# Performance work log

Measured on AMD Instinct MI355X. Metric: run time of the kernel, lower is better.

The kernel has to match this reference:

```python
import jax, jax.numpy as jnp
import numpy as np


def setup_inputs() -> dict:
    key = jax.random.key(0)
    k0, k1, k2, k3 = jax.random.split(key, 4)
    T, H, I, E, K = 2048, 2048, 1408, 8, 2  # tokens, hidden, intermediate, experts, top-k
    hidden_states = jax.random.normal(k0, (T, H), dtype=jnp.float32)
    router_weight = jax.random.normal(k1, (H, E), dtype=jnp.float32) * 0.02
    gate_up_weight = jax.random.normal(k2, (E, H, 2 * I), dtype=jnp.float32) * 0.02
    down_weight = jax.random.normal(k3, (E, I, H), dtype=jnp.float32) * 0.02
    return {
        "hidden_states": hidden_states,
        "router_weight": router_weight,
        "gate_up_weight": gate_up_weight,
        "down_weight": down_weight,
        "top_k": K,
    }


def reference(hidden_states, router_weight, gate_up_weight, down_weight, top_k):
    # Router: logits -> softmax -> top-k -> renormalize ('normalization' path)
    router_logits = hidden_states @ router_weight                  # [T, E]
    router_weights = jax.nn.softmax(router_logits, axis=-1)       # [T, E]
    topk_w, topk_idx = jax.lax.top_k(router_weights, top_k)       # [T, K]
    topk_w = topk_w / jnp.sum(topk_w, axis=-1, keepdims=True)     # router_weights_topk_reduced

    T, H = hidden_states.shape
    I = down_weight.shape[1]

    # Grouped gate_up GEMM (dense-per-expert reference for the grouped GMM)
    gate_up = jnp.einsum('th,ehf->etf', hidden_states, gate_up_weight)  # [E, T, 2I]
    gate, up = gate_up[..., :I], gate_up[..., I:]
    swish_out = jax.nn.silu(gate) * up                              # SWIGLU  [E, T, I]
    mlp_out = jnp.einsum('eti,eih->eth', swish_out, down_weight)    # [E, T, H]

    # Scatter-combine: gather each token's top-k expert outputs, weighted sum
    sel = mlp_out[topk_idx, jnp.arange(T)[:, None]]                 # [T, K, H]
    out = jnp.sum(sel * topk_w[..., None], axis=1)                  # [T, H]
    return out
```

## Files before the change

kernel.cpp:

```cpp
#include <hip/hip_runtime.h>
#include <hip/hip_bf16.h>
#include <math.h>

#define T_TOK 2048
#define HDIM  2048
#define IDIM  1408
#define NG    2816
#define NEXP  8
#define NPAIR (T_TOK*2)
#define RPAD  6144

typedef __attribute__((ext_vector_type(4))) float  f32x4;
typedef __attribute__((ext_vector_type(4))) short  s16x4;
typedef __attribute__((ext_vector_type(8))) short  s16x8;
typedef __attribute__((ext_vector_type(8))) __bf16 bf16x8;

__device__ __forceinline__ short f2bf(float f) {
  union { float f; unsigned u; } v; v.f = f;
  unsigned r = v.u + 0x7FFFu + ((v.u >> 16) & 1u);
  return (short)(r >> 16);
}

__device__ __forceinline__ float bf2f(short s) {
  union { unsigned u; float f; } v; v.u = ((unsigned)(unsigned short)s) << 16;
  return v.f;
}

__device__ __forceinline__ void gload_lds16(const void* g, void* l) {
  __builtin_amdgcn_global_load_lds((const __attribute__((address_space(1))) unsigned int*)g,
                                   (__attribute__((address_space(3))) unsigned int*)l,
                                   16, 0, 0);
}

__global__ void router_kernel(const float* __restrict__ hs, const float* __restrict__ rw,
                              int* __restrict__ pair_e, float* __restrict__ pair_w,
                              int* __restrict__ pair_pos, int* __restrict__ counts) {
  int wid = threadIdx.x >> 6, lane = threadIdx.x & 63;
  int t = blockIdx.x * 4 + wid;
  float acc[NEXP];
#pragma unroll
  for (int e = 0; e < NEXP; e++) acc[e] = 0.f;
  const float* h = hs + (size_t)t * HDIM;
  for (int k = lane; k < HDIM; k += 64) {
    float x = h[k];
    f32x4 w0 = *(const f32x4*)(rw + (size_t)k * NEXP);
    f32x4 w1 = *(const f32x4*)(rw + (size_t)k * NEXP + 4);
#pragma unroll
    for (int e = 0; e < 4; e++) { acc[e] += x * w0[e]; acc[e + 4] += x * w1[e]; }
  }
#pragma unroll
  for (int e = 0; e < NEXP; e++)
#pragma unroll
    for (int off = 32; off > 0; off >>= 1)
      acc[e] += __shfl_xor(acc[e], off, 64);
  if (lane == 0) {
    int i1 = 0; float v1 = acc[0];
#pragma unroll
    for (int e = 1; e < NEXP; e++) if (acc[e] > v1) { v1 = acc[e]; i1 = e; }
    int i2 = -1; float v2 = -3.4e38f;
#pragma unroll
    for (int e = 0; e < NEXP; e++) if (e != i1 && acc[e] > v2) { v2 = acc[e]; i2 = e; }
    float w2 = 1.f / (1.f + expf(v1 - v2));
    float w1 = 1.f - w2;
    int p1 = atomicAdd(&counts[i1], 1);
    int p2 = atomicAdd(&counts[i2], 1);
    pair_e[2*t]   = i1; pair_w[2*t]   = w1; pair_pos[2*t]   = p1;
    pair_e[2*t+1] = i2; pair_w[2*t+1] = w2; pair_pos[2*t+1] = p2;
  }
}

__global__ void prefix_kernel(const int* __restrict__ counts, int* __restrict__ offs) {
  if (threadIdx.x == 0) {
    int s = 0;
    for (int e = 0; e < NEXP; e++) { offs[e] = s; s += (counts[e] + 255) & ~255; }
    offs[NEXP] = s;
  }
}

__global__ void rowmap_kernel(const int* __restrict__ pair_e, const float* __restrict__ pair_w,
                              const int* __restrict__ pair_pos, const int* __restrict__ offs,
                              int* __restrict__ row_token, float* __restrict__ row_weight,
                              int* __restrict__ tok2row) {
  int p = blockIdx.x * 256 + threadIdx.x;
  if (p >= NPAIR) return;
  int e = pair_e[p];
  int row = offs[e] + pair_pos[p];
  row_token[row] = p >> 1;
  row_weight[row] = pair_w[p];
  tok2row[p] = row;
}

__global__ __launch_bounds__(256) void gather_kernel(const float* __restrict__ hs,
                                                     const int* __restrict__ row_token,
                                                     short* __restrict__ A_c) {
  int r = blockIdx.x;
  int tok = row_token[r];
  int t = threadIdx.x;
  if (tok < 0) {
    *(s16x8*)&A_c[(size_t)r * HDIM + t * 8] = (s16x8)0;
    return;
  }
  const float* src = hs + (size_t)tok * HDIM + t * 8;
  f32x4 v0 = *(const f32x4*)src;
  f32x4 v1 = *(const f32x4*)(src + 4);
  s16x8 o;
#pragma unroll
  for (int j = 0; j < 4; j++) { o[j] = f2bf(v0[j]); o[4 + j] = f2bf(v1[j]); }
  int dstg = (t & ~7) | ((t & 7) ^ (r & 7));
  *(s16x8*)&A_c[(size_t)r * HDIM + dstg * 8] = o;
}

__global__ __launch_bounds__(256) void convert_w_kernel(
    const float* __restrict__ src, short* __restrict__ dst, int K, int N) {
  int e = blockIdx.z;
  src += (size_t)e * K * N;
  dst += (size_t)e * K * N;
  int n0 = blockIdx.x * 64, k0 = blockIdx.y * 64;
  __shared__ short tile[64 * 76];
  int tid = threadIdx.x;
#pragma unroll
  for (int it = 0; it < 4; it++) {
    int s = tid + it * 256;
    int kk = s >> 4, nn = (s & 15) * 4;
    f32x4 v = *(const f32x4*)(src + (size_t)(k0 + kk) * N + n0 + nn);
    s16x4 b;
#pragma unroll
    for (int j = 0; j < 4; j++) b[j] = f2bf(v[j]);
    *(s16x4*)&tile[kk * 76 + nn] = b;
  }
  __syncthreads();
#pragma unroll
  for (int it = 0; it < 2; it++) {
    int s = tid + it * 256;
    int n = s >> 3, g = s & 7;
    int gs = g ^ (n & 7);
    s16x8 o;
#pragma unroll
    for (int j = 0; j < 8; j++) o[j] = tile[(gs * 8 + j) * 76 + n];
    *(s16x8*)&dst[(size_t)(n0 + n) * K + k0 + g * 8] = o;
  }
}

__global__ __launch_bounds__(512, 2) void gateup_kernel(
    const short* __restrict__ A_c, const float* __restrict__ guw,
    const int* __restrict__ offs, short* __restrict__ S) {
  int nb = blockIdx.x;
  int rb = blockIdx.y * 256;
  if (rb >= offs[NEXP]) return;
  int e = 0;
#pragma unroll
  for (int i = 1; i < NEXP; i++) e += (rb >= offs[i]);
  const float* Wsrc = guw + (size_t)e * HDIM * NG;
  const short* Ar = A_c + (size_t)rb * HDIM;

  __shared__ short bufA[2][256 * 64];
  __shared__ short bufB[256 * 64];
  int tid = threadIdx.x, lane = tid & 63, wid = tid >> 6;
  int wm = wid >> 2, wn = wid & 3;
  int lm = lane & 15, lg = lane >> 4;

  int oct = tid >> 4, kq = tid & 15;
  int n0 = oct * 8;
  int col = (n0 < 128) ? (nb * 128 + n0) : (IDIM + nb * 128 + (n0 - 128));
  const float* Bp = Wsrc + col;

  f32x4 acc[8][4];
#pragma unroll
  for (int a = 0; a < 8; a++)
#pragma unroll
    for (int b = 0; b < 4; b++) acc[a][b] = (f32x4)0.f;

  f32x4 va[4], vb[4];

  auto STAGE_A = [&](int buf, int kt) {
    int k0 = kt * 64;
#pragma unroll
    for (int it = 0; it < 4; it++) {
      int idx = tid + it * 512;
      gload_lds16(Ar + (size_t)(idx >> 3) * HDIM + k0 + (idx & 7) * 8, &bufA[buf][idx * 8]);
    }
  };
  auto LOAD_B = [&](int kt) {
    const float* p = Bp + (size_t)(kt * 64 + kq * 4) * NG;
#pragma unroll
    for (int j = 0; j < 4; j++) {
      va[j] = *(const f32x4*)(p + (size_t)j * NG);
      vb[j] = *(const f32x4*)(p + (size_t)j * NG + 4);
    }
  };
  auto WRITE_B = [&]() {
    int gc = kq >> 1, half = kq & 1;
#pragma unroll
    for (int i = 0; i < 8; i++) {
      int n = n0 + i;
      s16x4 w;
#pragma unroll
      for (int j = 0; j < 4; j++) w[j] = f2bf(i < 4 ? va[j][i] : vb[j][i - 4]);
      *(s16x4*)&bufB[n * 64 + ((gc ^ (n & 7)) * 8) + half * 4] = w;
    }
  };

  STAGE_A(0, 0);
  LOAD_B(0);
  const int NT = HDIM / 64;
#pragma unroll 1
  for (int kt = 0; kt < NT; kt++) {
    int cur = kt & 1;
    if (kt + 1 < NT) {
      STAGE_A(cur ^ 1, kt + 1);
      asm volatile("s_waitcnt vmcnt(4)" ::: "memory");
    } else {
      asm volatile("s_waitcnt vmcnt(0)" ::: "memory");
    }
    WRITE_B();
    if (kt + 1 < NT) LOAD_B(kt + 1);
    asm volatile("s_waitcnt lgkmcnt(0)" ::: "memory");
    __builtin_amdgcn_s_barrier();
#pragma unroll
    for (int ks = 0; ks < 2; ks++) {
      bf16x8 a[8], b[4];
#pragma unroll
      for (int mi = 0; mi < 8; mi++) {
        int m = wm * 128 + mi * 16 + lm;
        a[mi] = *(const bf16x8*)&bufA[cur][m * 64 + (((ks * 4 + lg) ^ (m & 7)) * 8)];
      }
#pragma unroll
      for (int nf = 0; nf < 4; nf++) {
        int n = (nf >> 1) * 128 + wn * 32 + (nf & 1) * 16 + lm;
        b[nf] = *(const bf16x8*)&bufB[n * 64 + (((ks * 4 + lg) ^ (n & 7)) * 8)];
      }
      __builtin_amdgcn_s_setprio(1);
#pragma unroll
      for (int mi = 0; mi < 8; mi++)
#pragma unroll
        for (int nf = 0; nf < 4; nf++)
          acc[mi][nf] = __builtin_amdgcn_mfma_f32_16x16x32_bf16(a[mi], b[nf], acc[mi][nf], 0, 0, 0);
      __builtin_amdgcn_s_setprio(0);
    }
    asm volatile("s_waitcnt lgkmcnt(0)" ::: "memory");
    __builtin_amdgcn_s_barrier();
  }
#pragma unroll
  for (int mi = 0; mi < 8; mi++)
#pragma unroll
    for (int nfg = 0; nfg < 2; nfg++)
#pragma unroll
      for (int j = 0; j < 4; j++) {
        int row = wm * 128 + mi * 16 + lg * 4 + j;
        int rg = rb + row;
        int scol = nb * 128 + wn * 32 + nfg * 16 + lm;
        int base = scol & ~63, o = scol & 63;
        int dc = (((o >> 3) ^ (rg & 7)) << 3) | (o & 7);
        float g = acc[mi][nfg][j], u = acc[mi][nfg + 2][j];
        float sv = (g / (1.f + expf(-g))) * u;
        S[(size_t)rg * IDIM + base + dc] = f2bf(sv);
      }
}

__global__ __launch_bounds__(512, 2) void down_kernel(
    const short* __restrict__ S, const short* __restrict__ W,
    const int* __restrict__ offs, short* __restrict__ Sout) {
  int nb = blockIdx.x;
  int rb = blockIdx.y * 256;
  if (rb >= offs[NEXP]) return;
  int e = 0;
#pragma unroll
  for (int i = 1; i < NEXP; i++) e += (rb >= offs[i]);
  const short* Ar = S + (size_t)rb * IDIM;
  const short* Bw = W + (size_t)e * HDIM * IDIM + (size_t)(nb * 256) * IDIM;

  __shared__ short As[2][256 * 64];
  __shared__ short Bs[2][256 * 64];
  int tid = threadIdx.x, lane = tid & 63, wid = tid >> 6;
  int wm = wid >> 2, wn = wid & 3;
  int lm = lane & 15, lg = lane >> 4;

  f32x4 acc[8][4];
#pragma unroll
  for (int a = 0; a < 8; a++)
#pragma unroll
    for (int b = 0; b < 4; b++) acc[a][b] = (f32x4)0.f;

  auto STAGE = [&](int buf, int kt) {
    int k0 = kt * 64;
#pragma unroll
    for (int it = 0; it < 4; it++) {
      int idx = tid + it * 512;
      gload_lds16(Ar + (size_t)(idx >> 3) * IDIM + k0 + (idx & 7) * 8, &As[buf][idx * 8]);
      gload_lds16(Bw + (size_t)(idx >> 3) * IDIM + k0 + (idx & 7) * 8, &Bs[buf][idx * 8]);
    }
  };
  auto READ_A = [&](bf16x8* dst, int buf, int mih, int ks) {
#pragma unroll
    for (int mi4 = 0; mi4 < 4; mi4++) {
      int m = wm * 128 + (mih * 4 + mi4) * 16 + lm;
      dst[mi4] = *(const bf16x8*)&As[buf][m * 64 + (((ks * 4 + lg) ^ (m & 7)) * 8)];
    }
  };
  auto READ_B = [&](bf16x8* dst, int buf, int ks) {
#pragma unroll
    for (int nf = 0; nf < 4; nf++) {
      int rbq = wn * 64 + nf * 16 + lm;
      dst[nf] = *(const bf16x8*)&Bs[buf][rbq * 64 + (((ks * 4 + lg) ^ (rbq & 7)) * 8)];
    }
  };
  auto MFMA16 = [&](const bf16x8* a, const bf16x8* b, int mih) {
    __builtin_amdgcn_s_setprio(1);
#pragma unroll
    for (int mi4 = 0; mi4 < 4; mi4++)
#pragma unroll
      for (int nf = 0; nf < 4; nf++)
        acc[mih * 4 + mi4][nf] =
            __builtin_amdgcn_mfma_f32_16x16x32_bf16(a[mi4], b[nf], acc[mih * 4 + mi4][nf], 0, 0, 0);
    __builtin_amdgcn_s_setprio(0);
  };

  STAGE(0, 0);
  const int NT = IDIM / 64;
#pragma unroll 1
  for (int kt = 0; kt < NT; kt++) {
    int cur = kt & 1;
    bf16x8 a0[4], a1[4], b0[4], b1[4];
    if (kt + 1 < NT) {
      STAGE(cur ^ 1, kt + 1);
      asm volatile("s_waitcnt vmcnt(8)" ::: "memory");
    } else {
      asm volatile("s_waitcnt vmcnt(0)" ::: "memory");
    }
    __builtin_amdgcn_s_barrier();
    READ_A(a0, cur, 0, 0); READ_B(b0, cur, 0);
    MFMA16(a0, b0, 0);
    READ_A(a1, cur, 1, 0);
    __builtin_amdgcn_s_barrier();
    MFMA16(a1, b0, 1);
    READ_A(a0, cur, 0, 1); READ_B(b1, cur, 1);
    __builtin_amdgcn_s_barrier();
    MFMA16(a0, b1, 0);
    READ_A(a1, cur, 1, 1);
    __builtin_amdgcn_s_barrier();
    MFMA16(a1, b1, 1);
    __builtin_amdgcn_s_barrier();
  }
#pragma unroll
  for (int mi = 0; mi < 8; mi++)
#pragma unroll
    for (int nf = 0; nf < 4; nf++)
#pragma unroll
      for (int j = 0; j < 4; j++) {
        int row = wm * 128 + mi * 16 + lg * 4 + j;
        int col = nb * 256 + wn * 64 + nf * 16 + lm;
        Sout[(size_t)(rb + row) * HDIM + col] = f2bf(acc[mi][nf][j]);
      }
}

__global__ __launch_bounds__(256) void combine_kernel(
    const short* __restrict__ Sout, const int* __restrict__ tok2row,
    const float* __restrict__ row_weight, float* __restrict__ out) {
  int t = blockIdx.x;
  int r1 = tok2row[2 * t], r2 = tok2row[2 * t + 1];
  float w1 = row_weight[r1], w2 = row_weight[r2];
  int c = threadIdx.x * 8;
  s16x8 a = *(const s16x8*)&Sout[(size_t)r1 * HDIM + c];
  s16x8 b = *(const s16x8*)&Sout[(size_t)r2 * HDIM + c];
  float* o = out + (size_t)t * HDIM + c;
#pragma unroll
  for (int j = 0; j < 8; j++) o[j] = w1 * bf2f(a[j]) + w2 * bf2f(b[j]);
}

extern "C" void kernel_launch(void* const* d_in, const int* in_sizes, int n_in,
                              void* d_out, int out_size, void* d_ws, size_t ws_size,
                              hipStream_t stream) {
  const float* hs  = (const float*)d_in[0];
  const float* rw  = (const float*)d_in[1];
  const float* guw = (const float*)d_in[2];
  const float* dw  = (const float*)d_in[3];
  float* out = (float*)d_out;

  char* ws = (char*)d_ws;
  size_t off = 0;
  auto take = [&](size_t b) { size_t p = off; off = (off + b + 255) & ~(size_t)255; return p; };
  size_t s_off      = take((size_t)RPAD * IDIM * 2);
  int*   counts     = (int*)(ws + take(32 * 4));
  int*   offs       = (int*)(ws + take(16 * 4));
  int*   pair_e     = (int*)(ws + take(NPAIR * 4));
  float* pair_w     = (float*)(ws + take(NPAIR * 4));
  int*   pair_pos   = (int*)(ws + take(NPAIR * 4));
  int*   row_token  = (int*)(ws + take(RPAD * 4));
  float* row_weight = (float*)(ws + take(RPAD * 4));
  int*   tok2row    = (int*)(ws + take(NPAIR * 4));
  size_t ac_off     = take((size_t)RPAD * HDIM * 2);
  size_t sout_off   = take((size_t)RPAD * HDIM * 2);
  size_t wd_off     = take((size_t)NEXP * HDIM * IDIM * 2);

  short* S    = (short*)(ws + s_off);
  short* A_c  = (short*)(ws + ac_off);
  short* Sout = (short*)(ws + sout_off);
  short* Wd   = (short*)(ws + wd_off);

  hipMemsetAsync(counts, 0, 32 * 4, stream);
  hipMemsetAsync(row_token, 0xFF, RPAD * 4, stream);

  router_kernel<<<T_TOK / 4, 256, 0, stream>>>(hs, rw, pair_e, pair_w, pair_pos, counts);
  prefix_kernel<<<1, 64, 0, stream>>>(counts, offs);
  rowmap_kernel<<<NPAIR / 256, 256, 0, stream>>>(pair_e, pair_w, pair_pos, offs,
                                                 row_token, row_weight, tok2row);
  gather_kernel<<<RPAD, 256, 0, stream>>>(hs, row_token, A_c);

  gateup_kernel<<<dim3(11, RPAD / 256), 512, 0, stream>>>(A_c, guw, offs, S);
  convert_w_kernel<<<dim3(HDIM / 64, IDIM / 64, NEXP), 256, 0, stream>>>(dw, Wd, IDIM, HDIM);
  down_kernel<<<dim3(8, RPAD / 256), 512, 0, stream>>>(S, Wd, offs, Sout);
  combine_kernel<<<T_TOK, 256, 0, stream>>>(Sout, tok2row, row_weight, out);
}
```

Measured before the change: 289.0 us.

## Fuse down-weight conversion into gate-up GEMM launch to overlap work

Measured after the change: 309.7 us. +7.1%, slower.

```diff
diff --git a/kernel.cpp b/kernel.cpp
--- a/kernel.cpp
+++ b/kernel.cpp
@@ -9,6 +9,9 @@
 #define NEXP  8
 #define NPAIR (T_TOK*2)
 #define RPAD  6144
+#define NB_GU   264
+#define NB_CVT  176
+#define CVT_TILES 32
 
 typedef __attribute__((ext_vector_type(4))) float  f32x4;
 typedef __attribute__((ext_vector_type(4))) short  s16x4;
@@ -110,42 +113,52 @@
   *(s16x8*)&A_c[(size_t)r * HDIM + dstg * 8] = o;
 }
 
-__global__ __launch_bounds__(256) void convert_w_kernel(
-    const float* __restrict__ src, short* __restrict__ dst, int K, int N) {
-  int e = blockIdx.z;
-  src += (size_t)e * K * N;
-  dst += (size_t)e * K * N;
-  int n0 = blockIdx.x * 64, k0 = blockIdx.y * 64;
-  __shared__ short tile[64 * 76];
+__global__ __launch_bounds__(512, 2) void gateup_cvt_kernel(
+    const short* __restrict__ A_c, const float* __restrict__ guw,
+    const float* __restrict__ dw, const int* __restrict__ offs,
+    short* __restrict__ S, short* __restrict__ Wd) {
+  __shared__ short bufA[2][256 * 64];
+  __shared__ short bufB[256 * 64];
+  int bid = blockIdx.x;
   int tid = threadIdx.x;
-#pragma unroll
-  for (int it = 0; it < 4; it++) {
-    int s = tid + it * 256;
-    int kk = s >> 4, nn = (s & 15) * 4;
-    f32x4 v = *(const f32x4*)(src + (size_t)(k0 + kk) * N + n0 + nn);
-    s16x4 b;
-#pragma unroll
-    for (int j = 0; j < 4; j++) b[j] = f2bf(v[j]);
-    *(s16x4*)&tile[kk * 76 + nn] = b;
-  }
-  __syncthreads();
-#pragma unroll
-  for (int it = 0; it < 2; it++) {
-    int s = tid + it * 256;
-    int n = s >> 3, g = s & 7;
-    int gs = g ^ (n & 7);
-    s16x8 o;
-#pragma unroll
-    for (int j = 0; j < 8; j++) o[j] = tile[(gs * 8 + j) * 76 + n];
-    *(s16x8*)&dst[(size_t)(n0 + n) * K + k0 + g * 8] = o;
-  }
-}
-
-__global__ __launch_bounds__(512, 2) void gateup_kernel(
-    const short* __restrict__ A_c, const float* __restrict__ guw,
-    const int* __restrict__ offs, short* __restrict__ S) {
-  int nb = blockIdx.x;
-  int rb = blockIdx.y * 256;
+
+  if (bid >= NB_GU) {
+    int c = bid - NB_GU;
+#pragma unroll 1
+    for (int i = 0; i < CVT_TILES; i++) {
+      int t = c * CVT_TILES + i;
+      int e = t / (32 * 22);
+      int rem = t % (32 * 22);
+      int ty = rem / 32, tx = rem % 32;
+      int k0 = ty * 64, n0 = tx * 64;
+      const float* src = dw + (size_t)e * IDIM * HDIM;
+#pragma unroll
+      for (int it = 0; it < 2; it++) {
+        int s = tid + it * 512;
+        int kk = s >> 4, nn = (s & 15) * 4;
+        f32x4 v = *(const f32x4*)(src + (size_t)(k0 + kk) * HDIM + n0 + nn);
+        s16x4 b;
+#pragma unroll
+        for (int j = 0; j < 4; j++) b[j] = f2bf(v[j]);
+        *(s16x4*)&bufB[kk * 76 + nn] = b;
+      }
+      __syncthreads();
+      {
+        int n = tid >> 3, g = tid & 7;
+        int gs = g ^ (n & 7);
+        s16x8 o;
+#pragma unroll
+        for (int j = 0; j < 8; j++) o[j] = bufB[(gs * 8 + j) * 76 + n];
+        *(s16x8*)&Wd[((size_t)e * HDIM + n0 + n) * IDIM + k0 + g * 8] = o;
+      }
+      __syncthreads();
+    }
+    return;
+  }
+
+  int nb = bid % 11;
+  int rblk = bid / 11;
+  int rb = rblk * 256;
   if (rb >= offs[NEXP]) return;
   int e = 0;
 #pragma unroll
@@ -153,9 +166,7 @@
   const float* Wsrc = guw + (size_t)e * HDIM * NG;
   const short* Ar = A_c + (size_t)rb * HDIM;
 
-  __shared__ short bufA[2][256 * 64];
-  __shared__ short bufB[256 * 64];
-  int tid = threadIdx.x, lane = tid & 63, wid = tid >> 6;
+  int lane = tid & 63, wid = tid >> 6;
   int wm = wid >> 2, wn = wid & 3;
   int lm = lane & 15, lg = lane >> 4;
 
@@ -406,8 +417,7 @@
                                                  row_token, row_weight, tok2row);
   gather_kernel<<<RPAD, 256, 0, stream>>>(hs, row_token, A_c);
 
-  gateup_kernel<<<dim3(11, RPAD / 256), 512, 0, stream>>>(A_c, guw, offs, S);
-  convert_w_kernel<<<dim3(HDIM / 64, IDIM / 64, NEXP), 256, 0, stream>>>(dw, Wd, IDIM, HDIM);
+  gateup_cvt_kernel<<<NB_GU + NB_CVT, 512, 0, stream>>>(A_c, guw, dw, offs, S, Wd);
   down_kernel<<<dim3(8, RPAD / 256), 512, 0, stream>>>(S, Wd, offs, Sout);
   combine_kernel<<<T_TOK, 256, 0, stream>>>(Sout, tok2row, row_weight, out);
 }
```

## Merge prefix into rowmap, fuse gather with weight convert, remap GEMM grids

Applied to the files above, without the earlier changes.

Measured after the change: 387.9 us. +34.2%, slower.

```diff
diff --git a/kernel.cpp b/kernel.cpp
--- a/kernel.cpp
+++ b/kernel.cpp
@@ -9,6 +9,7 @@
 #define NEXP  8
 #define NPAIR (T_TOK*2)
 #define RPAD  6144
+#define NCVT  (32*22*NEXP)
 
 typedef __attribute__((ext_vector_type(4))) float  f32x4;
 typedef __attribute__((ext_vector_type(4))) short  s16x4;
@@ -69,60 +70,66 @@
   }
 }
 
-__global__ void prefix_kernel(const int* __restrict__ counts, int* __restrict__ offs) {
+__global__ __launch_bounds__(256) void rowmap2_kernel(
+    const int* __restrict__ counts, const int* __restrict__ pair_e,
+    const float* __restrict__ pair_w, const int* __restrict__ pair_pos,
+    int* __restrict__ offs, int* __restrict__ row_token,
+    float* __restrict__ row_weight, int* __restrict__ tok2row) {
+  __shared__ int soffs[NEXP];
   if (threadIdx.x == 0) {
     int s = 0;
-    for (int e = 0; e < NEXP; e++) { offs[e] = s; s += (counts[e] + 255) & ~255; }
-    offs[NEXP] = s;
-  }
-}
-
-__global__ void rowmap_kernel(const int* __restrict__ pair_e, const float* __restrict__ pair_w,
-                              const int* __restrict__ pair_pos, const int* __restrict__ offs,
-                              int* __restrict__ row_token, float* __restrict__ row_weight,
-                              int* __restrict__ tok2row) {
+    for (int e = 0; e < NEXP; e++) { soffs[e] = s; s += (counts[e] + 255) & ~255; }
+    if (blockIdx.x == 0) {
+      for (int e = 0; e < NEXP; e++) offs[e] = soffs[e];
+      offs[NEXP] = s;
+    }
+  }
+  __syncthreads();
   int p = blockIdx.x * 256 + threadIdx.x;
   if (p >= NPAIR) return;
   int e = pair_e[p];
-  int row = offs[e] + pair_pos[p];
+  int row = soffs[e] + pair_pos[p];
   row_token[row] = p >> 1;
   row_weight[row] = pair_w[p];
   tok2row[p] = row;
 }
 
-__global__ __launch_bounds__(256) void gather_kernel(const float* __restrict__ hs,
-                                                     const int* __restrict__ row_token,
-                                                     short* __restrict__ A_c) {
-  int r = blockIdx.x;
-  int tok = row_token[r];
-  int t = threadIdx.x;
-  if (tok < 0) {
-    *(s16x8*)&A_c[(size_t)r * HDIM + t * 8] = (s16x8)0;
+__global__ __launch_bounds__(256) void gather_cvt_kernel(
+    const float* __restrict__ hs, const int* __restrict__ row_token,
+    short* __restrict__ A_c, const float* __restrict__ dw,
+    short* __restrict__ Wd) {
+  __shared__ short tile[64 * 76];
+  int bid = blockIdx.x, t = threadIdx.x;
+
+  if (bid < RPAD) {
+    int r = bid;
+    int tok = row_token[r];
+    if (tok < 0) {
+      *(s16x8*)&A_c[(size_t)r * HDIM + t * 8] = (s16x8)0;
+      return;
+    }
+    const float* src = hs + (size_t)tok * HDIM + t * 8;
+    f32x4 v0 = *(const f32x4*)src;
+    f32x4 v1 = *(const f32x4*)(src + 4);
+    s16x8 o;
+#pragma unroll
+    for (int j = 0; j < 4; j++) { o[j] = f2bf(v0[j]); o[4 + j] = f2bf(v1[j]); }
+    int dstg = (t & ~7) | ((t & 7) ^ (r & 7));
+    *(s16x8*)&A_c[(size_t)r * HDIM + dstg * 8] = o;
     return;
   }
-  const float* src = hs + (size_t)tok * HDIM + t * 8;
-  f32x4 v0 = *(const f32x4*)src;
-  f32x4 v1 = *(const f32x4*)(src + 4);
-  s16x8 o;
-#pragma unroll
-  for (int j = 0; j < 4; j++) { o[j] = f2bf(v0[j]); o[4 + j] = f2bf(v1[j]); }
-  int dstg = (t & ~7) | ((t & 7) ^ (r & 7));
-  *(s16x8*)&A_c[(size_t)r * HDIM + dstg * 8] = o;
-}
-
-__global__ __launch_bounds__(256) void convert_w_kernel(
-    const float* __restrict__ src, short* __restrict__ dst, int K, int N) {
-  int e = blockIdx.z;
-  src += (size_t)e * K * N;
-  dst += (size_t)e * K * N;
-  int n0 = blockIdx.x * 64, k0 = blockIdx.y * 64;
-  __shared__ short tile[64 * 76];
-  int tid = threadIdx.x;
+
+  int cid = bid - RPAD;
+  int e = cid / (32 * 22);
+  int rem = cid % (32 * 22);
+  int k0 = (rem / 32) * 64, n0 = (rem % 32) * 64;
+  const float* src = dw + (size_t)e * IDIM * HDIM;
+  short* dst = Wd + (size_t)e * IDIM * HDIM;
 #pragma unroll
   for (int it = 0; it < 4; it++) {
-    int s = tid + it * 256;
+    int s = t + it * 256;
     int kk = s >> 4, nn = (s & 15) * 4;
-    f32x4 v = *(const f32x4*)(src + (size_t)(k0 + kk) * N + n0 + nn);
+    f32x4 v = *(const f32x4*)(src + (size_t)(k0 + kk) * HDIM + n0 + nn);
     s16x4 b;
 #pragma unroll
     for (int j = 0; j < 4; j++) b[j] = f2bf(v[j]);
@@ -131,21 +138,22 @@
   __syncthreads();
 #pragma unroll
   for (int it = 0; it < 2; it++) {
-    int s = tid + it * 256;
+    int s = t + it * 256;
     int n = s >> 3, g = s & 7;
     int gs = g ^ (n & 7);
     s16x8 o;
 #pragma unroll
     for (int j = 0; j < 8; j++) o[j] = tile[(gs * 8 + j) * 76 + n];
-    *(s16x8*)&dst[(size_t)(n0 + n) * K + k0 + g * 8] = o;
+    *(s16x8*)&dst[(size_t)(n0 + n) * IDIM + k0 + g * 8] = o;
   }
 }
 
 __global__ __launch_bounds__(512, 2) void gateup_kernel(
     const short* __restrict__ A_c, const float* __restrict__ guw,
     const int* __restrict__ offs, short* __restrict__ S) {
-  int nb = blockIdx.x;
-  int rb = blockIdx.y * 256;
+  int bid = blockIdx.x;
+  int rblk = bid % 24, nb = bid / 24;
+  int rb = rblk * 256;
   if (rb >= offs[NEXP]) return;
   int e = 0;
 #pragma unroll
@@ -260,8 +268,9 @@
 __global__ __launch_bounds__(512, 2) void down_kernel(
     const short* __restrict__ S, const short* __restrict__ W,
     const int* __restrict__ offs, short* __restrict__ Sout) {
-  int nb = blockIdx.x;
-  int rb = blockIdx.y * 256;
+  int bid = blockIdx.x;
+  int rblk = bid % 24, nb = bid / 24;
+  int rb = rblk * 256;
   if (rb >= offs[NEXP]) return;
   int e = 0;
 #pragma unroll
@@ -401,13 +410,11 @@
   hipMemsetAsync(row_token, 0xFF, RPAD * 4, stream);
 
   router_kernel<<<T_TOK / 4, 256, 0, stream>>>(hs, rw, pair_e, pair_w, pair_pos, counts);
-  prefix_kernel<<<1, 64, 0, stream>>>(counts, offs);
-  rowmap_kernel<<<NPAIR / 256, 256, 0, stream>>>(pair_e, pair_w, pair_pos, offs,
-                                                 row_token, row_weight, tok2row);
-  gather_kernel<<<RPAD, 256, 0, stream>>>(hs, row_token, A_c);
-
-  gateup_kernel<<<dim3(11, RPAD / 256), 512, 0, stream>>>(A_c, guw, offs, S);
-  convert_w_kernel<<<dim3(HDIM / 64, IDIM / 64, NEXP), 256, 0, stream>>>(dw, Wd, IDIM, HDIM);
-  down_kernel<<<dim3(8, RPAD / 256), 512, 0, stream>>>(S, Wd, offs, Sout);
+  rowmap2_kernel<<<NPAIR / 256, 256, 0, stream>>>(counts, pair_e, pair_w, pair_pos,
+                                                  offs, row_token, row_weight, tok2row);
+  gather_cvt_kernel<<<RPAD + NCVT, 256, 0, stream>>>(hs, row_token, A_c, dw, Wd);
+
+  gateup_kernel<<<264, 512, 0, stream>>>(A_c, guw, offs, S);
+  down_kernel<<<192, 512, 0, stream>>>(S, Wd, offs, Sout);
   combine_kernel<<<T_TOK, 256, 0, stream>>>(Sout, tok2row, row_weight, out);
 }
```
